# Optimization experiments

Hardware: AMD Instinct MI355X
Metric: run time of the kernel (lower is better)

## Reference

```python
import jax, jax.numpy as jnp
import numpy as np

N_NODES = 50000
N_EDGES = 600000
IC, H, OC = 64, 128, 32
EPS = 1e-5


def setup_inputs() -> dict:
    key = jax.random.key(0)
    ks = jax.random.split(key, 8)
    x = jax.random.normal(ks[0], (N_NODES, IC), dtype=jnp.float32)
    ei = jax.random.randint(ks[1], (2, N_EDGES), 0, N_NODES, dtype=jnp.int64)
    proj_w = jax.random.normal(ks[2], (IC, H), dtype=jnp.float32) * 0.05
    proj_b = jnp.zeros((H,), dtype=jnp.float32)
    # conv_w[layer, lin, :, :] with lin order: key, query, value, skip
    conv_w = jax.random.normal(ks[3], (3, 4, H, H), dtype=jnp.float32) * 0.05
    conv_b = jnp.zeros((3, 4, H), dtype=jnp.float32)
    bn_gamma = jnp.ones((3, H), dtype=jnp.float32)
    bn_beta = jnp.zeros((3, H), dtype=jnp.float32)
    head_w = jax.random.normal(ks[4], (H, OC), dtype=jnp.float32) * 0.05
    head_b = jnp.zeros((OC,), dtype=jnp.float32)
    return {"x": x, "ei": ei, "proj_w": proj_w, "proj_b": proj_b,
            "conv_w": conv_w, "conv_b": conv_b, "bn_gamma": bn_gamma,
            "bn_beta": bn_beta, "head_w": head_w, "head_b": head_b}


def _res_gated_conv(x, src, dst, w, b):
    # PyG ResGatedGraphConv: out_i = skip(x_i) + sum_j sigmoid(key(x_i)+query(x_j)) * value(x_j)
    k = x @ w[0] + b[0]      # key   (applied to target/dst)
    q = x @ w[1] + b[1]      # query (applied to source/src)
    v = x @ w[2] + b[2]      # value (applied to source/src)
    msg = jax.nn.sigmoid(k[dst] + q[src]) * v[src]          # [E, H]
    agg = jax.ops.segment_sum(msg, dst, num_segments=x.shape[0])  # [N, H]
    return x @ w[3] + b[3] + agg


def _batchnorm(x, gamma, beta):
    # training-mode BatchNorm1d: batch statistics over the node dimension
    mean = jnp.mean(x, axis=0)
    var = jnp.var(x, axis=0)
    return gamma * (x - mean) * jax.lax.rsqrt(var + EPS) + beta


def reference(x, ei, proj_w, proj_b, conv_w, conv_b, bn_gamma, bn_beta, head_w, head_b):
    src, dst = ei[0], ei[1]
    h = jax.nn.relu(x @ proj_w + proj_b)
    for layer in range(3):
        h = _res_gated_conv(h, src, dst, conv_w[layer], conv_b[layer])
        h = jax.nn.relu(_batchnorm(h, bn_gamma[layer], bn_beta[layer]))
        # dropout(p=0.2) is identity in eval mode
    return h @ head_w + head_b
```

## Files before the change

### kernel.cpp

```cpp
#include <hip/hip_runtime.h>
#include <hip/hip_bf16.h>
#include <math.h>

#define HDIM 128
#define ICDIM 64
#define OCDIM 32
#define BN_EPS 1e-5f
#define NCH 64

typedef __attribute__((ext_vector_type(8))) short bv8;
typedef __attribute__((ext_vector_type(4))) float fv4;

static __device__ __forceinline__ unsigned short f2bf(float v) {
    __hip_bfloat16 t = __float2bfloat16(v);
    return *(unsigned short*)&t;
}
static __device__ __forceinline__ float bflo(unsigned int u) {
    union { unsigned int i; float f; } c; c.i = u << 16; return c.f;
}
static __device__ __forceinline__ float bfhi(unsigned int u) {
    union { unsigned int i; float f; } c; c.i = u & 0xffff0000u; return c.f;
}
static __device__ __forceinline__ unsigned int pack2bf(float a, float b) {
    return (unsigned int)f2bf(a) | ((unsigned int)f2bf(b) << 16);
}

__global__ void wconv_kernel(const float* __restrict__ src,
                             __hip_bfloat16* __restrict__ dst) {
    int mat = blockIdx.x;
    const float* s = src + (size_t)mat * HDIM * HDIM;
    __hip_bfloat16* d = dst + (size_t)mat * HDIM * HDIM;
    for (int idx = threadIdx.x; idx < HDIM * HDIM; idx += 256) {
        int i = idx >> 7, o = idx & 127;
        d[(size_t)o * HDIM + i] = __float2bfloat16(s[idx]);
    }
}

__global__ void wpconv_kernel(const float* __restrict__ src,
                              __hip_bfloat16* __restrict__ dst) {
    for (int idx = threadIdx.x; idx < ICDIM * HDIM; idx += 256) {
        int i = idx >> 7, o = idx & 127;
        dst[(size_t)o * ICDIM + i] = __float2bfloat16(src[idx]);
    }
}

__global__ __launch_bounds__(256)
void proj_mfma_kernel(const float* __restrict__ x,
                      const __hip_bfloat16* __restrict__ wp,
                      const float* __restrict__ b,
                      __hip_bfloat16* __restrict__ h, int n) {
    __shared__ unsigned int xs[NCH * ICDIM / 2];
    int tid = threadIdx.x;
    int m0 = blockIdx.x * NCH;

    const float2* xsrc = (const float2*)(x + (size_t)m0 * ICDIM);
    for (int i = tid; i < NCH * ICDIM / 2; i += 256) {
        int node = m0 + (i >> 5);
        float2 v = (node < n) ? xsrc[i] : (float2){0.f, 0.f};
        xs[i] = pack2bf(v.x, v.y);
    }

    int wv = tid >> 6;
    int lane = tid & 63;
    int j = lane & 15;
    int kg = lane >> 4;

    bv8 af[2][2];
#pragma unroll
    for (int gs = 0; gs < 2; ++gs)
#pragma unroll
        for (int ks = 0; ks < 2; ++ks)
            af[gs][ks] = *(const bv8*)((const unsigned short*)wp +
                (size_t)(wv * 32 + gs * 16 + j) * ICDIM + ks * 32 + kg * 8);

    float4 bias0 = *(const float4*)(b + wv * 32 + kg * 4);
    float4 bias1 = *(const float4*)(b + wv * 32 + 16 + kg * 4);

    __syncthreads();

#pragma unroll
    for (int t4 = 0; t4 < NCH / 16; ++t4) {
        const unsigned short* xrow =
            (const unsigned short*)xs + (t4 * 16 + j) * ICDIM + kg * 8;
        fv4 acc0 = (fv4){0.f, 0.f, 0.f, 0.f};
        fv4 acc1 = (fv4){0.f, 0.f, 0.f, 0.f};
#pragma unroll
        for (int ks = 0; ks < 2; ++ks) {
            bv8 bf = *(const bv8*)(xrow + ks * 32);
            acc0 = __builtin_amdgcn_mfma_f32_16x16x32_bf16(af[0][ks], bf, acc0, 0, 0, 0);
            acc1 = __builtin_amdgcn_mfma_f32_16x16x32_bf16(af[1][ks], bf, acc1, 0, 0, 0);
        }
        int node = m0 + t4 * 16 + j;
        if (node < n) {
            unsigned short* o =
                (unsigned short*)h + (size_t)node * HDIM + wv * 32 + kg * 4;
            ushort4 r0, r1;
            r0.x = f2bf(fmaxf(acc0.x + bias0.x, 0.f));
            r0.y = f2bf(fmaxf(acc0.y + bias0.y, 0.f));
            r0.z = f2bf(fmaxf(acc0.z + bias0.z, 0.f));
            r0.w = f2bf(fmaxf(acc0.w + bias0.w, 0.f));
            r1.x = f2bf(fmaxf(acc1.x + bias1.x, 0.f));
            r1.y = f2bf(fmaxf(acc1.y + bias1.y, 0.f));
            r1.z = f2bf(fmaxf(acc1.z + bias1.z, 0.f));
            r1.w = f2bf(fmaxf(acc1.w + bias1.w, 0.f));
            *(ushort4*)o = r0;
            *(ushort4*)(o + 16) = r1;
        }
    }
}

__global__ __launch_bounds__(1024)
void gemm4_fused_kernel(const __hip_bfloat16* __restrict__ hB,
                        const float* __restrict__ Ssrc,
                        const float* __restrict__ stp,
                        const float* __restrict__ gma,
                        const float* __restrict__ bta,
                        const __hip_bfloat16* __restrict__ wt4,
                        const float* __restrict__ b4,
                        __hip_bfloat16* __restrict__ K,
                        unsigned int* __restrict__ QV,
                        float* __restrict__ S, int n) {
    __shared__ unsigned short hs[NCH * HDIM];
    int tid = threadIdx.x;
    int m0 = blockIdx.x * NCH;

    if (Ssrc) {
        const float4* src = (const float4*)(Ssrc + (size_t)m0 * HDIM);
        float4 v0 = src[tid * 2];
        float4 v1 = src[tid * 2 + 1];
        int c0 = (tid * 8) & 127;
        float invn = 1.f / (float)n;
        float vv[8] = {v0.x, v0.y, v0.z, v0.w, v1.x, v1.y, v1.z, v1.w};
        unsigned int* dst = (unsigned int*)hs + tid * 4;
#pragma unroll
        for (int p = 0; p < 8; p += 2) {
            int c = c0 + p;
            float mA = stp[c] * invn, mB = stp[c + 1] * invn;
            float scA = gma[c] * rsqrtf(stp[128 + c] * invn - mA * mA + BN_EPS);
            float scB = gma[c + 1] * rsqrtf(stp[129 + c] * invn - mB * mB + BN_EPS);
            float shA = bta[c] - mA * scA, shB = bta[c + 1] - mB * scB;
            float rA = fmaxf(fmaf(vv[p], scA, shA), 0.f);
            float rB = fmaxf(fmaf(vv[p + 1], scB, shB), 0.f);
            dst[p >> 1] = pack2bf(rA, rB);
        }
    } else {
        const uint4* src = (const uint4*)((const unsigned short*)hB + (size_t)m0 * HDIM);
        ((uint4*)hs)[tid] = src[tid];
    }

    int wv = tid >> 6;
    int lane = tid & 63;
    int lin = wv >> 2;
    int g2 = wv & 3;
    int j = lane & 15;
    int kg = lane >> 4;

    const unsigned short* wbase =
        (const unsigned short*)(wt4 + (size_t)lin * HDIM * HDIM);
    bv8 af[2][4];
#pragma unroll
    for (int gs = 0; gs < 2; ++gs)
#pragma unroll
        for (int ks = 0; ks < 4; ++ks)
            af[gs][ks] = *(const bv8*)(wbase +
                (size_t)(g2 * 32 + gs * 16 + j) * HDIM + ks * 32 + kg * 8);

    const float* bl = b4 + lin * HDIM;
    float4 bias0 = *(const float4*)(bl + g2 * 32 + kg * 4);
    float4 bias1 = *(const float4*)(bl + g2 * 32 + 16 + kg * 4);

    __syncthreads();

#pragma unroll
    for (int t4 = 0; t4 < NCH / 16; ++t4) {
        const unsigned short* hrow = hs + (t4 * 16 + j) * HDIM + kg * 8;
        fv4 acc0 = (fv4){0.f, 0.f, 0.f, 0.f};
        fv4 acc1 = (fv4){0.f, 0.f, 0.f, 0.f};
#pragma unroll
        for (int ks = 0; ks < 4; ++ks) {
            bv8 bf = *(const bv8*)(hrow + ks * 32);
            acc0 = __builtin_amdgcn_mfma_f32_16x16x32_bf16(af[0][ks], bf, acc0, 0, 0, 0);
            acc1 = __builtin_amdgcn_mfma_f32_16x16x32_bf16(af[1][ks], bf, acc1, 0, 0, 0);
        }
        int node = m0 + t4 * 16 + j;
        if (node >= n) continue;
        int c0 = g2 * 32 + kg * 4;
        float f0 = acc0.x + bias0.x, f1 = acc0.y + bias0.y;
        float f2 = acc0.z + bias0.z, f3 = acc0.w + bias0.w;
        float f4 = acc1.x + bias1.x, f5 = acc1.y + bias1.y;
        float f6 = acc1.z + bias1.z, f7 = acc1.w + bias1.w;
        if (lin == 3) {
            float* o = S + (size_t)node * HDIM + c0;
            *(float4*)o = (float4){f0, f1, f2, f3};
            *(float4*)(o + 16) = (float4){f4, f5, f6, f7};
        } else if (lin == 0) {
            unsigned short* o = (unsigned short*)K + (size_t)node * HDIM + c0;
            *(ushort4*)o = (ushort4){f2bf(f0), f2bf(f1), f2bf(f2), f2bf(f3)};
            *(ushort4*)(o + 16) = (ushort4){f2bf(f4), f2bf(f5), f2bf(f6), f2bf(f7)};
        } else {
            unsigned int* o = QV + (size_t)node * HDIM + c0 + (lin - 1);
            o[0] = pack2bf(f0, f1);
            o[2] = pack2bf(f2, f3);
            o[16] = pack2bf(f4, f5);
            o[18] = pack2bf(f6, f7);
        }
    }
}

__global__ void hist_kernel(const int* __restrict__ ei, int* __restrict__ deg, int e) {
    int i = blockIdx.x * 256 + threadIdx.x;
    if (i < e) atomicAdd(&deg[ei[(size_t)e + i]], 1);
}

__global__ void scan1_kernel(const int* __restrict__ deg, int* __restrict__ incl,
                             int* __restrict__ bsum, int n) {
    __shared__ int tmp[256];
    int i = blockIdx.x * 256 + threadIdx.x;
    int v = (i < n) ? deg[i] : 0;
    tmp[threadIdx.x] = v;
    __syncthreads();
    for (int ofs = 1; ofs < 256; ofs <<= 1) {
        int t = (threadIdx.x >= ofs) ? tmp[threadIdx.x - ofs] : 0;
        __syncthreads();
        tmp[threadIdx.x] += t;
        __syncthreads();
    }
    if (i < n) incl[i] = tmp[threadIdx.x];
    if (threadIdx.x == 255) bsum[blockIdx.x] = tmp[255];
}

__global__ void scan2_kernel(int* __restrict__ bsum, int nb) {
    __shared__ int tmp[256];
    int v = (threadIdx.x < nb) ? bsum[threadIdx.x] : 0;
    tmp[threadIdx.x] = v;
    __syncthreads();
    for (int ofs = 1; ofs < 256; ofs <<= 1) {
        int t = (threadIdx.x >= ofs) ? tmp[threadIdx.x - ofs] : 0;
        __syncthreads();
        tmp[threadIdx.x] += t;
        __syncthreads();
    }
    if (threadIdx.x < nb) bsum[threadIdx.x] = tmp[threadIdx.x] - v;
}

__global__ void scan3_kernel(const int* __restrict__ deg, const int* __restrict__ incl,
                             const int* __restrict__ bsum, int* __restrict__ off,
                             int* __restrict__ cursor, int n, int e) {
    int i = blockIdx.x * 256 + threadIdx.x;
    if (i < n) {
        int ex = incl[i] - deg[i] + bsum[blockIdx.x];
        off[i] = ex;
        cursor[i] = ex;
        if (i == n - 1) off[n] = e;
    }
}

__global__ void scatter_kernel(const int* __restrict__ ei, int* __restrict__ cursor,
                               int* __restrict__ esrc, int e) {
    int i = blockIdx.x * 256 + threadIdx.x;
    if (i < e) {
        int dst = ei[(size_t)e + i];
        int pos = atomicAdd(&cursor[dst], 1);
        esrc[pos] = ei[i];
    }
}

__global__ void agg_kernel(const int* __restrict__ off, const int* __restrict__ esrc,
                           const __hip_bfloat16* __restrict__ kb,
                           const unsigned int* __restrict__ QV,
                           float* __restrict__ S, int n) {
    int d = blockIdx.x * 4 + (threadIdx.x >> 6);
    if (d >= n) return;
    int lane = threadIdx.x & 63;
    const uint2* qvw = (const uint2*)QV;
    unsigned int kwu = ((const unsigned int*)kb)[(size_t)d * 64 + lane];
    float k0 = bflo(kwu), k1 = bfhi(kwu);
    float a0 = 0.f, a1 = 0.f;

#define EDGE(u)                                               \
    {                                                         \
        float g0 = k0 + bflo(u.x), g1 = k1 + bfhi(u.x);       \
        float e0 = __expf(-g0), e1 = __expf(-g1);             \
        a0 += __fdividef(bflo(u.y), 1.f + e0);                \
        a1 += __fdividef(bfhi(u.y), 1.f + e1);                \
    }

    int j = off[d], s1 = off[d + 1];
    for (; j + 4 <= s1; j += 4) {
        int sA = esrc[j], sB = esrc[j + 1], sC = esrc[j + 2], sD = esrc[j + 3];
        uint2 uA = qvw[(size_t)sA * 64 + lane];
        uint2 uB = qvw[(size_t)sB * 64 + lane];
        uint2 uC = qvw[(size_t)sC * 64 + lane];
        uint2 uD = qvw[(size_t)sD * 64 + lane];
        EDGE(uA); EDGE(uB); EDGE(uC); EDGE(uD);
    }
    for (; j < s1; ++j) {
        int s = esrc[j];
        uint2 u = qvw[(size_t)s * 64 + lane];
        EDGE(u);
    }
#undef EDGE

    float2* sp = (float2*)(S + (size_t)d * HDIM) + lane;
    float2 old = *sp;
    old.x += a0; old.y += a1;
    *sp = old;
}

__global__ void stats_kernel(const float* __restrict__ s,
                             float* __restrict__ stats, int n) {
    int c = threadIdx.x & 127, rh = threadIdx.x >> 7;
    int r0 = blockIdx.x * 128;
    int r1 = min(r0 + 128, n);
    float sum = 0.f, sq = 0.f;
    for (int r = r0 + rh; r < r1; r += 2) {
        float v = s[(size_t)r * HDIM + c];
        sum += v;
        sq = fmaf(v, v, sq);
    }
    __shared__ float ls[2][HDIM], lq[2][HDIM];
    ls[rh][c] = sum;
    lq[rh][c] = sq;
    __syncthreads();
    if (rh == 0) {
        atomicAdd(&stats[c], ls[0][c] + ls[1][c]);
        atomicAdd(&stats[HDIM + c], lq[0][c] + lq[1][c]);
    }
}

__global__ void head_bn_kernel(const float* __restrict__ S,
                               const float* __restrict__ stats,
                               const float* __restrict__ gamma,
                               const float* __restrict__ beta,
                               const float* __restrict__ w,
                               const float* __restrict__ b,
                               float* __restrict__ out, int n) {
    __shared__ float hsm[8][HDIM];
    float invn = 1.f / (float)n;
    for (int i = threadIdx.x; i < 8 * HDIM; i += 256) {
        int r = i >> 7, c = i & 127;
        int node = blockIdx.x * 8 + r;
        float v = 0.f;
        if (node < n) {
            float mean = stats[c] * invn;
            float var = stats[128 + c] * invn - mean * mean;
            float sc = gamma[c] * rsqrtf(var + BN_EPS);
            float sh = beta[c] - mean * sc;
            v = fmaxf(fmaf(S[(size_t)node * HDIM + c], sc, sh), 0.f);
        }
        hsm[r][c] = v;
    }
    __syncthreads();
    int c = threadIdx.x & 31;
    int ng = threadIdx.x >> 5;
    int node = blockIdx.x * 8 + ng;
    if (node >= n) return;
    float acc = b[c];
#pragma unroll
    for (int k = 0; k < HDIM; ++k)
        acc = fmaf(hsm[ng][k], w[k * OCDIM + c], acc);
    out[(size_t)node * OCDIM + c] = acc;
}

extern "C" void kernel_launch(void* const* d_in, const int* in_sizes, int n_in,
                              void* d_out, int out_size, void* d_ws, size_t ws_size,
                              hipStream_t stream) {
    const float* x      = (const float*)d_in[0];
    const int*   ei     = (const int*)  d_in[1];
    const float* proj_w = (const float*)d_in[2];
    const float* proj_b = (const float*)d_in[3];
    const float* conv_w = (const float*)d_in[4];
    const float* conv_b = (const float*)d_in[5];
    const float* bn_g   = (const float*)d_in[6];
    const float* bn_b   = (const float*)d_in[7];
    const float* head_w = (const float*)d_in[8];
    const float* head_b = (const float*)d_in[9];
    float* out = (float*)d_out;

    int n = in_sizes[0] / ICDIM;
    int e = in_sizes[1] / 2;

    size_t nh = (size_t)n * HDIM;
    size_t need = nh * 4 + 768 * 4 + nh * 2 + nh * 2 + nh * 4
                + (size_t)12 * HDIM * HDIM * 2 + (size_t)HDIM * ICDIM * 2
                + ((size_t)3 * n + (n + 1) + 256 + e) * 4;
    if (ws_size < need) return;

    float* S  = (float*)d_ws;
    float* st = S + nh;
    __hip_bfloat16* h = (__hip_bfloat16*)(st + 768);
    __hip_bfloat16* K = h + nh;
    unsigned int* QV = (unsigned int*)(K + nh);
    __hip_bfloat16* Wt = (__hip_bfloat16*)(QV + nh);
    __hip_bfloat16* Wp = Wt + (size_t)12 * HDIM * HDIM;

    int* deg    = (int*)(Wp + (size_t)HDIM * ICDIM);
    int* incl   = deg + n;
    int* off    = incl + n;
    int* cursor = off + n + 1;
    int* bsum   = cursor + n;
    int* esrc   = bsum + 256;

    hipMemsetAsync(st, 0, 768 * sizeof(float), stream);
    hipMemsetAsync(deg, 0, (size_t)n * sizeof(int), stream);

    int gb_e = (e + 255) / 256;
    int gb_n = (n + 255) / 256;

    wconv_kernel<<<12, 256, 0, stream>>>(conv_w, Wt);
    wpconv_kernel<<<1, 256, 0, stream>>>(proj_w, Wp);
    proj_mfma_kernel<<<(n + NCH - 1) / NCH, 256, 0, stream>>>(x, Wp, proj_b, h, n);

    hist_kernel<<<gb_e, 256, 0, stream>>>(ei, deg, e);
    scan1_kernel<<<gb_n, 256, 0, stream>>>(deg, incl, bsum, n);
    scan2_kernel<<<1, 256, 0, stream>>>(bsum, gb_n);
    scan3_kernel<<<gb_n, 256, 0, stream>>>(deg, incl, bsum, off, cursor, n, e);
    scatter_kernel<<<gb_e, 256, 0, stream>>>(ei, cursor, esrc, e);

    int gm = (n + NCH - 1) / NCH;
    for (int l = 0; l < 3; ++l) {
        const float* Ssrc = (l == 0) ? nullptr : S;
        const float* stp  = (l == 0) ? st : st + (size_t)(l - 1) * 256;
        const float* gma  = (l == 0) ? bn_g : bn_g + (size_t)(l - 1) * HDIM;
        const float* bta  = (l == 0) ? bn_b : bn_b + (size_t)(l - 1) * HDIM;
        gemm4_fused_kernel<<<gm, 1024, 0, stream>>>(
            h, Ssrc, stp, gma, bta,
            Wt + (size_t)l * 4 * HDIM * HDIM, conv_b + (size_t)l * 4 * HDIM,
            K, QV, S, n);
        agg_kernel<<<(n + 3) / 4, 256, 0, stream>>>(off, esrc, K, QV, S, n);
        stats_kernel<<<(n + 127) / 128, 256, 0, stream>>>(S, st + l * 256, n);
    }

    head_bn_kernel<<<(n + 7) / 8, 256, 0, stream>>>(
        S, st + 2 * 256, bn_g + 2 * HDIM, bn_b + 2 * HDIM, head_w, head_b, out, n);
}
```

Baseline: 496.9 us.

## Swizzle LDS layouts, software-pipeline edge gathers, merge weight prep kernels

The node tiles in LDS used by the projection and fused 4-way GEMM kernels are now stored with an XOR swizzle on 16-byte chunks, so the MFMA B-operand reads avoid bank conflicts. The edge aggregation loop now prefetches the next group of four QV gathers before computing the current group, to overlap gather latency with the sigmoid math. The two weight conversion kernels are merged into one launch. The prefetch costs extra registers, and the swizzle adds address arithmetic.

```diff
diff --git a/kernel.cpp b/kernel.cpp
--- a/kernel.cpp
+++ b/kernel.cpp
@@ -25,22 +25,23 @@
     return (unsigned int)f2bf(a) | ((unsigned int)f2bf(b) << 16);
 }
 
-__global__ void wconv_kernel(const float* __restrict__ src,
-                             __hip_bfloat16* __restrict__ dst) {
+__global__ void wprep_kernel(const float* __restrict__ conv_w,
+                             const float* __restrict__ proj_w,
+                             __hip_bfloat16* __restrict__ Wt,
+                             __hip_bfloat16* __restrict__ Wp) {
     int mat = blockIdx.x;
-    const float* s = src + (size_t)mat * HDIM * HDIM;
-    __hip_bfloat16* d = dst + (size_t)mat * HDIM * HDIM;
-    for (int idx = threadIdx.x; idx < HDIM * HDIM; idx += 256) {
-        int i = idx >> 7, o = idx & 127;
-        d[(size_t)o * HDIM + i] = __float2bfloat16(s[idx]);
-    }
-}
-
-__global__ void wpconv_kernel(const float* __restrict__ src,
-                              __hip_bfloat16* __restrict__ dst) {
-    for (int idx = threadIdx.x; idx < ICDIM * HDIM; idx += 256) {
-        int i = idx >> 7, o = idx & 127;
-        dst[(size_t)o * ICDIM + i] = __float2bfloat16(src[idx]);
+    if (mat < 12) {
+        const float* s = conv_w + (size_t)mat * HDIM * HDIM;
+        __hip_bfloat16* d = Wt + (size_t)mat * HDIM * HDIM;
+        for (int idx = threadIdx.x; idx < HDIM * HDIM; idx += 256) {
+            int i = idx >> 7, o = idx & 127;
+            d[(size_t)o * HDIM + i] = __float2bfloat16(s[idx]);
+        }
+    } else {
+        for (int idx = threadIdx.x; idx < ICDIM * HDIM; idx += 256) {
+            int i = idx >> 7, o = idx & 127;
+            Wp[(size_t)o * ICDIM + i] = __float2bfloat16(proj_w[idx]);
+        }
     }
 }
 
@@ -57,13 +58,14 @@
     for (int i = tid; i < NCH * ICDIM / 2; i += 256) {
         int node = m0 + (i >> 5);
         float2 v = (node < n) ? xsrc[i] : (float2){0.f, 0.f};
-        xs[i] = pack2bf(v.x, v.y);
+        xs[i ^ (((i >> 5) & 7) << 2)] = pack2bf(v.x, v.y);
     }
 
     int wv = tid >> 6;
     int lane = tid & 63;
     int j = lane & 15;
     int kg = lane >> 4;
+    int sw = (j & 7) << 4;
 
     bv8 af[2][2];
 #pragma unroll
@@ -80,13 +82,12 @@
 
 #pragma unroll
     for (int t4 = 0; t4 < NCH / 16; ++t4) {
-        const unsigned short* xrow =
-            (const unsigned short*)xs + (t4 * 16 + j) * ICDIM + kg * 8;
+        const char* rowbase = (const char*)xs + (t4 * 16 + j) * (ICDIM * 2);
         fv4 acc0 = (fv4){0.f, 0.f, 0.f, 0.f};
         fv4 acc1 = (fv4){0.f, 0.f, 0.f, 0.f};
 #pragma unroll
         for (int ks = 0; ks < 2; ++ks) {
-            bv8 bf = *(const bv8*)(xrow + ks * 32);
+            bv8 bf = *(const bv8*)(rowbase + ((kg * 16 + ks * 64) ^ sw));
             acc0 = __builtin_amdgcn_mfma_f32_16x16x32_bf16(af[0][ks], bf, acc0, 0, 0, 0);
             acc1 = __builtin_amdgcn_mfma_f32_16x16x32_bf16(af[1][ks], bf, acc1, 0, 0, 0);
         }
@@ -123,6 +124,7 @@
     __shared__ unsigned short hs[NCH * HDIM];
     int tid = threadIdx.x;
     int m0 = blockIdx.x * NCH;
+    int wsw = ((tid >> 4) & 7) << 4;
 
     if (Ssrc) {
         const float4* src = (const float4*)(Ssrc + (size_t)m0 * HDIM);
@@ -131,7 +133,7 @@
         int c0 = (tid * 8) & 127;
         float invn = 1.f / (float)n;
         float vv[8] = {v0.x, v0.y, v0.z, v0.w, v1.x, v1.y, v1.z, v1.w};
-        unsigned int* dst = (unsigned int*)hs + tid * 4;
+        unsigned int* dst = (unsigned int*)((char*)hs + ((tid * 16) ^ wsw));
 #pragma unroll
         for (int p = 0; p < 8; p += 2) {
             int c = c0 + p;
@@ -145,7 +147,7 @@
         }
     } else {
         const uint4* src = (const uint4*)((const unsigned short*)hB + (size_t)m0 * HDIM);
-        ((uint4*)hs)[tid] = src[tid];
+        *(uint4*)((char*)hs + ((tid * 16) ^ wsw)) = src[tid];
     }
 
     int wv = tid >> 6;
@@ -154,6 +156,7 @@
     int g2 = wv & 3;
     int j = lane & 15;
     int kg = lane >> 4;
+    int sw = (j & 7) << 4;
 
     const unsigned short* wbase =
         (const unsigned short*)(wt4 + (size_t)lin * HDIM * HDIM);
@@ -173,12 +176,12 @@
 
 #pragma unroll
     for (int t4 = 0; t4 < NCH / 16; ++t4) {
-        const unsigned short* hrow = hs + (t4 * 16 + j) * HDIM + kg * 8;
+        const char* rowbase = (const char*)hs + (t4 * 16 + j) * (HDIM * 2);
         fv4 acc0 = (fv4){0.f, 0.f, 0.f, 0.f};
         fv4 acc1 = (fv4){0.f, 0.f, 0.f, 0.f};
 #pragma unroll
         for (int ks = 0; ks < 4; ++ks) {
-            bv8 bf = *(const bv8*)(hrow + ks * 32);
+            bv8 bf = *(const bv8*)(rowbase + ((kg * 16 + ks * 64) ^ sw));
             acc0 = __builtin_amdgcn_mfma_f32_16x16x32_bf16(af[0][ks], bf, acc0, 0, 0, 0);
             acc1 = __builtin_amdgcn_mfma_f32_16x16x32_bf16(af[1][ks], bf, acc1, 0, 0, 0);
         }
@@ -285,16 +288,28 @@
         a1 += __fdividef(bfhi(u.y), 1.f + e1);                \
     }
 
-    int j = off[d], s1 = off[d + 1];
-    for (; j + 4 <= s1; j += 4) {
-        int sA = esrc[j], sB = esrc[j + 1], sC = esrc[j + 2], sD = esrc[j + 3];
-        uint2 uA = qvw[(size_t)sA * 64 + lane];
-        uint2 uB = qvw[(size_t)sB * 64 + lane];
-        uint2 uC = qvw[(size_t)sC * 64 + lane];
-        uint2 uD = qvw[(size_t)sD * 64 + lane];
-        EDGE(uA); EDGE(uB); EDGE(uC); EDGE(uD);
-    }
-    for (; j < s1; ++j) {
+    int j0 = off[d], s1 = off[d + 1];
+    int nb = (s1 - j0) >> 2;
+    uint2 cu0, cu1, cu2, cu3;
+    if (nb > 0) {
+        int sA = esrc[j0], sB = esrc[j0 + 1], sC = esrc[j0 + 2], sD = esrc[j0 + 3];
+        cu0 = qvw[(size_t)sA * 64 + lane];
+        cu1 = qvw[(size_t)sB * 64 + lane];
+        cu2 = qvw[(size_t)sC * 64 + lane];
+        cu3 = qvw[(size_t)sD * 64 + lane];
+    }
+    for (int b = 1; b < nb; ++b) {
+        int jn = j0 + b * 4;
+        int sA = esrc[jn], sB = esrc[jn + 1], sC = esrc[jn + 2], sD = esrc[jn + 3];
+        uint2 nu0 = qvw[(size_t)sA * 64 + lane];
+        uint2 nu1 = qvw[(size_t)sB * 64 + lane];
+        uint2 nu2 = qvw[(size_t)sC * 64 + lane];
+        uint2 nu3 = qvw[(size_t)sD * 64 + lane];
+        EDGE(cu0); EDGE(cu1); EDGE(cu2); EDGE(cu3);
+        cu0 = nu0; cu1 = nu1; cu2 = nu2; cu3 = nu3;
+    }
+    if (nb > 0) { EDGE(cu0); EDGE(cu1); EDGE(cu2); EDGE(cu3); }
+    for (int j = j0 + nb * 4; j < s1; ++j) {
         int s = esrc[j];
         uint2 u = qvw[(size_t)s * 64 + lane];
         EDGE(u);
@@ -407,8 +422,7 @@
     int gb_e = (e + 255) / 256;
     int gb_n = (n + 255) / 256;
 
-    wconv_kernel<<<12, 256, 0, stream>>>(conv_w, Wt);
-    wpconv_kernel<<<1, 256, 0, stream>>>(proj_w, Wp);
+    wprep_kernel<<<13, 256, 0, stream>>>(conv_w, proj_w, Wt, Wp);
     proj_mfma_kernel<<<(n + NCH - 1) / NCH, 256, 0, stream>>>(x, Wp, proj_b, h, n);
 
     hist_kernel<<<gb_e, 256, 0, stream>>>(ei, deg, e);
```

Result: no change. 495.9 us (-0.2%).
